# Kernel optimization log

Measured on AMD Instinct MI355X. Metric: run time of the kernel, lower is better.

The kernel has to match this reference:

```python
import jax, jax.numpy as jnp
import numpy as np

EMBED_DIM = 1024
N_TOKENS = 8192


def setup_inputs() -> dict:
    key = jax.random.key(0)
    k1, k2, k3 = jax.random.split(key, 3)
    inputs = jax.random.normal(k1, (N_TOKENS, EMBED_DIM), dtype=jnp.float32)
    rotation_params = jax.random.normal(k2, (EMBED_DIM, EMBED_DIM), dtype=jnp.float32)
    entangle_params = jax.random.normal(k3, (EMBED_DIM, EMBED_DIM), dtype=jnp.float32)
    return {"inputs": inputs, "rotation_params": rotation_params, "entangle_params": entangle_params}


def reference(inputs, rotation_params, entangle_params):
    # query/key projections from externally supplied params
    embed_dim = inputs.shape[-1]
    wq = rotation_params.reshape(embed_dim, -1)
    wk = entangle_params.reshape(embed_dim, -1)
    query = inputs @ wq          # [N, d]
    key = inputs @ wk            # [N, d]
    scale = 1.0 / jnp.sqrt(jnp.float32(embed_dim))
    scores = jax.nn.softmax(jnp.einsum('nd,md->nm', query, key) * scale, axis=-1)  # [N, N]
    context = scores @ inputs    # attend over raw inputs (V = inputs)
    return context
```

## Files before the change

kernel.cpp:

```cpp
#include <hip/hip_runtime.h>
#include <hip/hip_bf16.h>


typedef _Float16 f16x8 __attribute__((ext_vector_type(8)));
typedef _Float16 f16x4 __attribute__((ext_vector_type(4)));
typedef float    f32x4 __attribute__((ext_vector_type(4)));

#define TM 128
#define TN 128

__device__ __forceinline__ void g2lds16(const _Float16* g, _Float16* l) {
    __builtin_amdgcn_global_load_lds(
        (__attribute__((address_space(1))) unsigned int*)(g),
        (__attribute__((address_space(3))) unsigned int*)(l),
        16, 0, 0);
}


__global__ __launch_bounds__(256) void split_rows(const float* __restrict__ src,
                                                  _Float16* __restrict__ hi,
                                                  _Float16* __restrict__ lo,
                                                  long n) {
    long i = (long)blockIdx.x * blockDim.x + threadIdx.x;
    long stride = (long)gridDim.x * blockDim.x;
    for (; i < n; i += stride) {
        float v = src[i];
        _Float16 h = (_Float16)v;
        hi[i] = h;
        lo[i] = (_Float16)(v - (float)h);
    }
}

__global__ void transpose_split(const float* __restrict__ src,
                                _Float16* __restrict__ dhi,
                                _Float16* __restrict__ dlo,
                                int R, int C) {
    __shared__ float tile[32][33];
    int c0 = blockIdx.x * 32, r0 = blockIdx.y * 32;
    int tx = threadIdx.x, ty = threadIdx.y;
#pragma unroll
    for (int k = 0; k < 4; ++k)
        tile[ty + 8 * k][tx] = src[(size_t)(r0 + ty + 8 * k) * C + c0 + tx];
    __syncthreads();
#pragma unroll
    for (int k = 0; k < 4; ++k) {
        float v = tile[tx][ty + 8 * k];
        _Float16 h = (_Float16)v;
        size_t idx = (size_t)(c0 + ty + 8 * k) * R + r0 + tx;
        dhi[idx] = h;
        if (dlo) dlo[idx] = (_Float16)(v - (float)h);
    }
}

__global__ __launch_bounds__(256) void add_rows(const float* __restrict__ a,
                                                const float* __restrict__ b,
                                                float* __restrict__ out, long n4) {
    long i = (long)blockIdx.x * blockDim.x + threadIdx.x;
    long stride = (long)gridDim.x * blockDim.x;
    for (; i < n4; i += stride) {
        float4 x = ((const float4*)a)[i];
        float4 y = ((const float4*)b)[i];
        x.x += y.x; x.y += y.y; x.z += y.z; x.w += y.w;
        ((float4*)out)[i] = x;
    }
}

template <int TERMS, int SPLIT_OUT, int SWAP, int BKH>
__global__ __launch_bounds__(256, TERMS == 3 ? 3 : 4) void gemm_bt(
    const _Float16* __restrict__ Ahi, const _Float16* __restrict__ Alo,
    const _Float16* __restrict__ Bhi, const _Float16* __restrict__ Blo,
    float* __restrict__ C, _Float16* __restrict__ Chi, _Float16* __restrict__ Clo,
    long lda, long ldb, long ldc, int K, long zA, long zB, long zC) {
    constexpr int NBUF = (TERMS == 3) ? 4 : 2;
    __shared__ __align__(16) _Float16 s[NBUF * 128 * BKH];

    const long z = blockIdx.z;
    Ahi += z * zA;
    Bhi += z * zB;
    if constexpr (TERMS == 3) { Alo += z * zA; Blo += z * zB; }
    if constexpr (SPLIT_OUT) { Chi += z * zC; Clo += z * zC; }
    else C += z * zC;

    const int t = threadIdx.x;
    const int wave = t >> 6;
    const int lane = t & 63;
    const int lm = lane & 15;
    const int lq = lane >> 4;
    const int wr = wave >> 1;
    const int wc = wave & 1;

    const long rowBase = (long)(SWAP ? blockIdx.x : blockIdx.y) * TM;
    const long colBase = (long)(SWAP ? blockIdx.y : blockIdx.x) * TN;

    const _Float16* src;
    long myLd, gRow0;
    int ldsBaseH;
    if constexpr (TERMS == 3) {
        const _Float16* a = (wave & 1) ? Alo : Ahi;
        const _Float16* b = (wave & 1) ? Blo : Bhi;
        src = (wave & 2) ? b : a;
        myLd = (wave & 2) ? ldb : lda;
        gRow0 = (wave & 2) ? colBase : rowBase;
        ldsBaseH = wave * (128 * BKH);
    } else {
        src = (wave & 2) ? Bhi : Ahi;
        myLd = (wave & 2) ? ldb : lda;
        gRow0 = ((wave & 2) ? colBase : rowBase) + (wave & 1) * 64;
        ldsBaseH = (wave >> 1) * (128 * BKH) + (wave & 1) * (64 * BKH);
    }
    constexpr int LPR = BKH / 8;
    constexpr int RPI = 64 / LPR;
    constexpr int NISS = (TERMS == 3 ? 128 : 64) / RPI;
    const int lr = lane / LPR;
    const int slot = lane % LPR;
    const int swzW = (BKH == 32) ? ((lr >> 1) & 3) : (lr & 7);
    const _Float16* rp = src + (gRow0 + lr) * myLd + (slot ^ swzW) * 8;
    _Float16* ldsW = &s[ldsBaseH];

    const _Float16* sAh = s;
    const _Float16* sBh = s + (TERMS == 3 ? 2 : 1) * 128 * BKH;
    const _Float16* sAl = s + 128 * BKH;
    const _Float16* sBl = s + 3 * 128 * BKH;

    const int swzR = (BKH == 32) ? ((lm >> 1) & 3) : (lm & 7);

    f32x4 acc[4][4];
#pragma unroll
    for (int r = 0; r < 4; ++r)
#pragma unroll
        for (int c = 0; c < 4; ++c)
#pragma unroll
            for (int i = 0; i < 4; ++i) acc[r][c][i] = 0.0f;

    for (int k0 = 0; k0 < K; k0 += BKH) {
        __syncthreads();
#pragma unroll
        for (int j = 0; j < NISS; ++j)
            g2lds16(rp + (long)(j * RPI) * myLd + k0, ldsW + j * 512);
        __syncthreads();

#pragma unroll
        for (int kk = 0; kk < BKH; kk += 32) {
            const int gb = kk >> 3;
            f16x8 ah[4], bh[4], al[4], bl[4];
#pragma unroll
            for (int r = 0; r < 4; ++r) {
                int ra = (wr * 64 + r * 16 + lm) * BKH + ((gb + lq) ^ swzR) * 8;
                int rb = (wc * 64 + r * 16 + lm) * BKH + ((gb + lq) ^ swzR) * 8;
                ah[r] = *(const f16x8*)&sAh[ra];
                bh[r] = *(const f16x8*)&sBh[rb];
                if constexpr (TERMS == 3) {
                    al[r] = *(const f16x8*)&sAl[ra];
                    bl[r] = *(const f16x8*)&sBl[rb];
                }
            }
#pragma unroll
            for (int r = 0; r < 4; ++r)
#pragma unroll
                for (int c = 0; c < 4; ++c) {
                    acc[r][c] = __builtin_amdgcn_mfma_f32_16x16x32_f16(
                        ah[r], bh[c], acc[r][c], 0, 0, 0);
                    if constexpr (TERMS == 3) {
                        acc[r][c] = __builtin_amdgcn_mfma_f32_16x16x32_f16(
                            ah[r], bl[c], acc[r][c], 0, 0, 0);
                        acc[r][c] = __builtin_amdgcn_mfma_f32_16x16x32_f16(
                            al[r], bh[c], acc[r][c], 0, 0, 0);
                    }
                }
        }
    }

#pragma unroll
    for (int r = 0; r < 4; ++r)
#pragma unroll
        for (int c = 0; c < 4; ++c)
#pragma unroll
            for (int i = 0; i < 4; ++i) {
                long row = rowBase + wr * 64 + r * 16 + lq * 4 + i;
                long col = colBase + wc * 64 + c * 16 + lm;
                if constexpr (SPLIT_OUT) {
                    float v = acc[r][c][i];
                    _Float16 h = (_Float16)v;
                    Chi[row * ldc + col] = h;
                    Clo[row * ldc + col] = (_Float16)(v - (float)h);
                } else {
                    C[row * ldc + col] = acc[r][c][i];
                }
            }
}

__global__ __launch_bounds__(256) void softmax_rows(const float* __restrict__ S,
                                                    _Float16* __restrict__ P,
                                                    long ldp, int N) {
    const int row = blockIdx.x;
    const int t = threadIdx.x;
    const float4* rowp = (const float4*)(S + (size_t)row * N);
    float4 v[8];
    float mx = -3.4e38f;
#pragma unroll
    for (int i = 0; i < 8; ++i) {
        v[i] = rowp[t + 256 * i];
        mx = fmaxf(mx, fmaxf(fmaxf(v[i].x, v[i].y), fmaxf(v[i].z, v[i].w)));
    }
    __shared__ float red[8];
#pragma unroll
    for (int off = 32; off >= 1; off >>= 1) mx = fmaxf(mx, __shfl_xor(mx, off));
    if ((t & 63) == 0) red[t >> 6] = mx;
    __syncthreads();
    mx = fmaxf(fmaxf(red[0], red[1]), fmaxf(red[2], red[3]));

    float sum = 0.0f;
#pragma unroll
    for (int i = 0; i < 8; ++i) {
        v[i].x = __expf((v[i].x - mx) * 0.03125f);
        v[i].y = __expf((v[i].y - mx) * 0.03125f);
        v[i].z = __expf((v[i].z - mx) * 0.03125f);
        v[i].w = __expf((v[i].w - mx) * 0.03125f);
        sum += (v[i].x + v[i].y) + (v[i].z + v[i].w);
    }
#pragma unroll
    for (int off = 32; off >= 1; off >>= 1) sum += __shfl_xor(sum, off);
    if ((t & 63) == 0) red[4 + (t >> 6)] = sum;
    __syncthreads();
    float inv = 1.0f / (red[4] + red[5] + red[6] + red[7]);

    f16x4* prow = (f16x4*)(P + (size_t)row * ldp);
#pragma unroll
    for (int i = 0; i < 8; ++i) {
        f16x4 o;
        o[0] = (_Float16)(v[i].x * inv);
        o[1] = (_Float16)(v[i].y * inv);
        o[2] = (_Float16)(v[i].z * inv);
        o[3] = (_Float16)(v[i].w * inv);
        prow[t + 256 * i] = o;
    }
}

extern "C" void kernel_launch(void* const* d_in, const int* in_sizes, int n_in,
                              void* d_out, int out_size, void* d_ws, size_t ws_size,
                              hipStream_t stream) {
    const float* X  = (const float*)d_in[0];
    const float* Wq = (const float*)d_in[1];
    const float* Wk = (const float*)d_in[2];
    float* out = (float*)d_out;

    const long Nt = 8192, D = 1024;
    char* ws = (char*)d_ws;
    const size_t MB = 1024ull * 1024ull;

    _Float16* XT  = (_Float16*)(ws + 0);
    _Float16* Qhi = (_Float16*)(ws + 16 * MB);
    _Float16* Qlo = (_Float16*)(ws + 32 * MB);
    _Float16* Khi = (_Float16*)(ws + 48 * MB);
    _Float16* Klo = (_Float16*)(ws + 64 * MB);
    _Float16* Xhi   = (_Float16*)(ws + 80 * MB);
    _Float16* Xlo   = (_Float16*)(ws + 96 * MB);
    _Float16* WqThi = (_Float16*)(ws + 112 * MB);
    _Float16* WqTlo = (_Float16*)(ws + 114 * MB);
    _Float16* WkThi = (_Float16*)(ws + 116 * MB);
    _Float16* WkTlo = (_Float16*)(ws + 118 * MB);
    float* PK0 = (float*)(ws + 16 * MB);

    const size_t rowBytes = (size_t)Nt * 4;
    const bool planA = ws_size >= 208 * MB + 128 * rowBytes;
    _Float16* Pbuf = (_Float16*)(ws + 80 * MB);
    float* Sc;
    long chunk;
    if (planA) {
        Sc = (float*)(ws + 208 * MB);
        size_t avail = ws_size - 208 * MB;
        chunk = (long)((avail / rowBytes / 128) * 128);
    } else {
        Sc = (float*)(ws + 80 * MB);
        size_t avail = ws_size > 80 * MB ? ws_size - 80 * MB : 0;
        chunk = (long)((avail / rowBytes / 128) * 128);
        if (chunk < 128) chunk = 128;
    }
    if (chunk > Nt) chunk = Nt;
    {
        long nch = (Nt + chunk - 1) / chunk;
        chunk = (((Nt + nch - 1) / nch) + 127) / 128 * 128;
    }

    transpose_split<<<dim3(32, 256), dim3(32, 8), 0, stream>>>(X, XT, nullptr,
                                                               (int)Nt, (int)D);
    split_rows<<<1024, 256, 0, stream>>>(X, Xhi, Xlo, Nt * D);
    transpose_split<<<dim3(32, 32), dim3(32, 8), 0, stream>>>(Wq, WqThi, WqTlo,
                                                              (int)D, (int)D);
    transpose_split<<<dim3(32, 32), dim3(32, 8), 0, stream>>>(Wk, WkThi, WkTlo,
                                                              (int)D, (int)D);

    gemm_bt<3, 1, 1, 32><<<dim3(Nt / TM, D / TN, 2), 256, 0, stream>>>(
        Xhi, Xlo, WqThi, WqTlo, nullptr, Qhi, Qlo, D, D, D, (int)D,
        0, (long)(4 * MB / 2), (long)(32 * MB / 2));

    long done = 0;
    while (done < Nt) {
        long cur = Nt - done < chunk ? Nt - done : chunk;
        gemm_bt<3, 0, 0, 32><<<dim3(Nt / TN, cur / TM, 1), 256, 0, stream>>>(
            Qhi + done * D, Qlo + done * D, Khi, Klo, Sc, nullptr, nullptr,
            D, D, Nt, (int)D, 0, 0, 0);
        if (planA) {
            softmax_rows<<<(int)cur, 256, 0, stream>>>(Sc, Pbuf + done * Nt,
                                                       Nt, (int)Nt);
        } else {
            softmax_rows<<<(int)cur, 256, 0, stream>>>(Sc, (_Float16*)Sc,
                                                       2 * Nt, (int)Nt);
            gemm_bt<1, 0, 1, 64><<<dim3(cur / TM, D / TN, 1), 256, 0, stream>>>(
                (const _Float16*)Sc, nullptr, XT, nullptr,
                out + done * D, nullptr, nullptr, 2 * Nt, Nt, D, (int)Nt,
                0, 0, 0);
        }
        done += cur;
    }

    if (planA) {
        gemm_bt<1, 0, 1, 64><<<dim3(Nt / TM, D / TN, 2), 256, 0, stream>>>(
            Pbuf, nullptr, XT, nullptr, PK0, nullptr, nullptr,
            Nt, Nt, D, (int)(Nt / 2),
            Nt / 2, Nt / 2, Nt * D);
        add_rows<<<1024, 256, 0, stream>>>(PK0, PK0 + Nt * D, out, Nt * D / 4);
    }
}
```

Before: 856.1 us.

## Switch GEMM inner loop to 32x32x16 MFMA tiles with 2x2 per-wave fragments

The GEMM kernel now uses the 32x32x16 f16 MFMA instruction with a 2x2 grid of 32x32 fragments per wave instead of a 4x4 grid of 16x16 tiles. This cuts the number of LDS fragment loads per MFMA and the instruction count, aiming to raise matrix-core throughput. The output index mapping is rewritten for the 32x32 accumulator layout. The PV GEMM launches also drop SWAP and transpose the grid so consecutive blocks walk along the column dimension, which changes L2 reuse patterns.

```diff
diff --git a/kernel.cpp b/kernel.cpp
--- a/kernel.cpp
+++ b/kernel.cpp
@@ -4,7 +4,7 @@
 
 typedef _Float16 f16x8 __attribute__((ext_vector_type(8)));
 typedef _Float16 f16x4 __attribute__((ext_vector_type(4)));
-typedef float    f32x4 __attribute__((ext_vector_type(4)));
+typedef float    f32x16 __attribute__((ext_vector_type(16)));
 
 #define TM 128
 #define TN 128
@@ -84,8 +84,8 @@
     const int t = threadIdx.x;
     const int wave = t >> 6;
     const int lane = t & 63;
-    const int lm = lane & 15;
-    const int lq = lane >> 4;
+    const int m32 = lane & 31;
+    const int kh = lane >> 5;
     const int wr = wave >> 1;
     const int wc = wave & 1;
 
@@ -122,15 +122,15 @@
     const _Float16* sAl = s + 128 * BKH;
     const _Float16* sBl = s + 3 * 128 * BKH;
 
-    const int swzR = (BKH == 32) ? ((lm >> 1) & 3) : (lm & 7);
-
-    f32x4 acc[4][4];
-#pragma unroll
-    for (int r = 0; r < 4; ++r)
-#pragma unroll
-        for (int c = 0; c < 4; ++c)
-#pragma unroll
-            for (int i = 0; i < 4; ++i) acc[r][c][i] = 0.0f;
+    const int swzR = (BKH == 32) ? ((m32 >> 1) & 3) : (m32 & 7);
+
+    f32x16 acc[2][2];
+#pragma unroll
+    for (int r = 0; r < 2; ++r)
+#pragma unroll
+        for (int c = 0; c < 2; ++c)
+#pragma unroll
+            for (int i = 0; i < 16; ++i) acc[r][c][i] = 0.0f;
 
     for (int k0 = 0; k0 < K; k0 += BKH) {
         __syncthreads();
@@ -140,13 +140,13 @@
         __syncthreads();
 
 #pragma unroll
-        for (int kk = 0; kk < BKH; kk += 32) {
-            const int gb = kk >> 3;
-            f16x8 ah[4], bh[4], al[4], bl[4];
-#pragma unroll
-            for (int r = 0; r < 4; ++r) {
-                int ra = (wr * 64 + r * 16 + lm) * BKH + ((gb + lq) ^ swzR) * 8;
-                int rb = (wc * 64 + r * 16 + lm) * BKH + ((gb + lq) ^ swzR) * 8;
+        for (int ks = 0; ks < BKH / 16; ++ks) {
+            const int grp = ks * 2 + kh;
+            f16x8 ah[2], bh[2], al[2], bl[2];
+#pragma unroll
+            for (int r = 0; r < 2; ++r) {
+                int ra = (wr * 64 + r * 32 + m32) * BKH + (grp ^ swzR) * 8;
+                int rb = (wc * 64 + r * 32 + m32) * BKH + (grp ^ swzR) * 8;
                 ah[r] = *(const f16x8*)&sAh[ra];
                 bh[r] = *(const f16x8*)&sBh[rb];
                 if constexpr (TERMS == 3) {
@@ -155,15 +155,15 @@
                 }
             }
 #pragma unroll
-            for (int r = 0; r < 4; ++r)
-#pragma unroll
-                for (int c = 0; c < 4; ++c) {
-                    acc[r][c] = __builtin_amdgcn_mfma_f32_16x16x32_f16(
+            for (int r = 0; r < 2; ++r)
+#pragma unroll
+                for (int c = 0; c < 2; ++c) {
+                    acc[r][c] = __builtin_amdgcn_mfma_f32_32x32x16_f16(
                         ah[r], bh[c], acc[r][c], 0, 0, 0);
                     if constexpr (TERMS == 3) {
-                        acc[r][c] = __builtin_amdgcn_mfma_f32_16x16x32_f16(
+                        acc[r][c] = __builtin_amdgcn_mfma_f32_32x32x16_f16(
                             ah[r], bl[c], acc[r][c], 0, 0, 0);
-                        acc[r][c] = __builtin_amdgcn_mfma_f32_16x16x32_f16(
+                        acc[r][c] = __builtin_amdgcn_mfma_f32_32x32x16_f16(
                             al[r], bh[c], acc[r][c], 0, 0, 0);
                     }
                 }
@@ -171,13 +171,14 @@
     }
 
 #pragma unroll
-    for (int r = 0; r < 4; ++r)
-#pragma unroll
-        for (int c = 0; c < 4; ++c)
-#pragma unroll
-            for (int i = 0; i < 4; ++i) {
-                long row = rowBase + wr * 64 + r * 16 + lq * 4 + i;
-                long col = colBase + wc * 64 + c * 16 + lm;
+    for (int r = 0; r < 2; ++r)
+#pragma unroll
+        for (int c = 0; c < 2; ++c)
+#pragma unroll
+            for (int i = 0; i < 16; ++i) {
+                long row = rowBase + wr * 64 + r * 32 +
+                           (i & 3) + 8 * (i >> 2) + 4 * kh;
+                long col = colBase + wc * 64 + c * 32 + m32;
                 if constexpr (SPLIT_OUT) {
                     float v = acc[r][c][i];
                     _Float16 h = (_Float16)v;
@@ -306,7 +307,7 @@
         } else {
             softmax_rows<<<(int)cur, 256, 0, stream>>>(Sc, (_Float16*)Sc,
                                                        2 * Nt, (int)Nt);
-            gemm_bt<1, 0, 1, 64><<<dim3(cur / TM, D / TN, 1), 256, 0, stream>>>(
+            gemm_bt<1, 0, 0, 64><<<dim3(D / TN, cur / TM, 1), 256, 0, stream>>>(
                 (const _Float16*)Sc, nullptr, XT, nullptr,
                 out + done * D, nullptr, nullptr, 2 * Nt, Nt, D, (int)Nt,
                 0, 0, 0);
@@ -315,7 +316,7 @@
     }
 
     if (planA) {
-        gemm_bt<1, 0, 1, 64><<<dim3(Nt / TM, D / TN, 2), 256, 0, stream>>>(
+        gemm_bt<1, 0, 0, 64><<<dim3(D / TN, Nt / TM, 2), 256, 0, stream>>>(
             Pbuf, nullptr, XT, nullptr, PK0, nullptr, nullptr,
             Nt, Nt, D, (int)(Nt / 2),
             Nt / 2, Nt / 2, Nt * D);
```

Result: slower. 913.1 us (+6.7%).
